# Performance work log

Hardware: AMD Instinct MI355X
Metric: run time of the kernel (lower is better)

## Reference

```python
import jax, jax.numpy as jnp
import numpy as np

E = 256   # in_features / embed_dim
O = 256   # out_features
H = 8     # n_heads
D = E // H  # head_dim
NEG = -1e9
SLOPE = 0.2  # leaky_relu negative slope


def setup_inputs() -> dict:
    key = jax.random.key(0)
    ks = jax.random.split(key, 9)
    B, N = 8, 1024
    x = jax.random.normal(ks[0], (B, N, E), dtype=jnp.float32)
    adj_matrix = jax.random.randint(ks[1], (N, N), 0, 2, dtype=jnp.int32)
    s = 1.0 / np.sqrt(E)
    w_in = jax.random.uniform(ks[2], (3 * E, E), jnp.float32, -s, s)   # packed q/k/v proj (torch in_proj_weight)
    b_in = jnp.zeros((3 * E,), jnp.float32)
    w_out = jax.random.uniform(ks[3], (E, E), jnp.float32, -s, s)      # MHA out_proj
    b_out = jnp.zeros((E,), jnp.float32)
    w_lin = jax.random.uniform(ks[4], (O, E), jnp.float32, -s, s)      # final nn.Linear
    b_lin = jax.random.uniform(ks[5], (O,), jnp.float32, -s, s)
    return {"x": x, "adj_matrix": adj_matrix, "w_in": w_in, "b_in": b_in,
            "w_out": w_out, "b_out": b_out, "w_lin": w_lin, "b_lin": b_lin}


def reference(x, adj_matrix, w_in, b_in, w_out, b_out, w_lin, b_lin):
    B, N, _ = x.shape
    scale = 1.0 / np.sqrt(D)
    qkv = x @ w_in.T + b_in                      # [B,N,3E]
    q, k, v = jnp.split(qkv, 3, axis=-1)
    q = q.reshape(B, N, H, D) * scale
    k = k.reshape(B, N, H, D)
    v = v.reshape(B, N, H, D)
    scores = jnp.einsum('bnhd,bmhd->bhnm', q, k)  # [B,H,N,N]
    allowed = (adj_matrix != 0)[None, None]       # mask True where adj==0 -> disallowed
    scores = jnp.where(allowed, scores, NEG)
    attn = jax.nn.softmax(scores, axis=-1)
    ctx = jnp.einsum('bhnm,bmhd->bnhd', attn, v).reshape(B, N, E)
    attended = ctx @ w_out.T + b_out              # MHA output (dropout is identity in eval)
    out = attended @ w_lin.T + b_lin
    return jnp.where(out >= 0, out, SLOPE * out)  # leaky_relu(0.2)
```

## Files before the change

### kernel.cpp

```cpp
#include <hip/hip_runtime.h>
#include <math.h>

#define EE 256
#define HH 8
#define DD 32
#define NB 8
#define NS 1024
#define SLOPE 0.2f

typedef float f32x4 __attribute__((ext_vector_type(4)));
typedef short short8 __attribute__((ext_vector_type(8)));

static __device__ __forceinline__ unsigned short f2b(float f) {
    unsigned int u = __float_as_uint(f);
    u = (u + 0x7FFFu + ((u >> 16) & 1u)) >> 16;
    return (unsigned short)u;
}

static __device__ __forceinline__ unsigned int cvtpk(float lo, float hi) {
    unsigned int r;
    asm("v_cvt_pk_bf16_f32 %0, %1, %2" : "=v"(r) : "v"(lo), "v"(hi));
    return r;
}

static __device__ __forceinline__ void gload_lds16(const void* g, void* l) {
    __builtin_amdgcn_global_load_lds(
        (const __attribute__((address_space(1))) unsigned int*)g,
        (__attribute__((address_space(3))) unsigned int*)l, 16, 0, 0);
}

__global__ __launch_bounds__(256) void cvt_all(const float* __restrict__ x,
                                               const float* __restrict__ wi,
                                               unsigned short* __restrict__ xb,
                                               unsigned short* __restrict__ wib) {
    int t = blockIdx.x * 256 + threadIdx.x;
    const float* src; unsigned short* dst; int base;
    if (t < 262144) { src = x;  dst = xb;  base = t; }
    else            { src = wi; dst = wib; base = t - 262144; }
    const float4* s = (const float4*)(src + (size_t)base * 8);
    float4 a = s[0], b = s[1];
    uint4 wv;
    wv.x = cvtpk(a.x, a.y); wv.y = cvtpk(a.z, a.w);
    wv.z = cvtpk(b.x, b.y); wv.w = cvtpk(b.z, b.w);
    *(uint4*)(dst + (size_t)base * 8) = wv;
}

__global__ __launch_bounds__(256) void make_comb(
    const float* __restrict__ wo, const float* __restrict__ bo,
    const float* __restrict__ wl, const float* __restrict__ bl,
    unsigned short* __restrict__ wcb, float* __restrict__ bcomb) {
    int o = blockIdx.x, c = threadIdx.x;
    const float* wlr = wl + (size_t)o * EE;
    float acc = 0.f;
#pragma unroll 8
    for (int e = 0; e < EE; ++e)
        acc = fmaf(wlr[e], wo[(size_t)e * EE + c], acc);
    wcb[(size_t)o * EE + c] = f2b(acc);
    if (c == 0) {
        float bb = bl[o];
        for (int e = 0; e < EE; ++e) bb = fmaf(wlr[e], bo[e], bb);
        bcomb[o] = bb;
    }
}

__global__ __launch_bounds__(256) void adj_to_bits(const int* __restrict__ adj,
                                                   unsigned int* __restrict__ bits) {
    int t = blockIdx.x * 256 + threadIdx.x;
    int n = t >> 5, w = t & 31;
    const int* p = adj + (size_t)n * NS + w * 32;
    unsigned int word = 0;
#pragma unroll
    for (int i = 0; i < 32; i += 4) {
        int4 a = *(const int4*)(p + i);
        if (a.x) word |= 1u << i;
        if (a.y) word |= 1u << (i + 1);
        if (a.z) word |= 1u << (i + 2);
        if (a.w) word |= 1u << (i + 3);
    }
    bits[t] = word;
}

template<int MODE>
__global__ __launch_bounds__(256) void gemm_mfma(
    const unsigned short* __restrict__ A, const unsigned short* __restrict__ W,
    const float* __restrict__ bias, void* __restrict__ out,
    unsigned short* __restrict__ qb, unsigned short* __restrict__ kb,
    unsigned short* __restrict__ vtb, int Nout) {
    __shared__ __align__(16) unsigned short As[128 * 64];
    __shared__ __align__(16) unsigned short Bs[64 * 64];
    int tid = threadIdx.x, w = tid >> 6, lane = tid & 63;
    int lq = lane & 15, g = lane >> 4;
    int wr = w >> 1, wc = w & 1;
    int m0 = blockIdx.y * 128, n0 = blockIdx.x * 64;
    int r8 = lane >> 3, c8 = (lane & 7) * 8;
    f32x4 acc[4][2];
#pragma unroll
    for (int i = 0; i < 4; ++i)
#pragma unroll
        for (int j = 0; j < 2; ++j) acc[i][j] = (f32x4){0.f, 0.f, 0.f, 0.f};

    for (int k0 = 0; k0 < 256; k0 += 64) {
        __syncthreads();
#pragma unroll
        for (int i = 0; i < 4; ++i)
            gload_lds16(A + (size_t)(m0 + w * 32 + i * 8 + r8) * 256 + k0 + c8,
                        &As[(w * 32 + i * 8) * 64]);
#pragma unroll
        for (int i = 0; i < 2; ++i)
            gload_lds16(W + (size_t)(n0 + w * 16 + i * 8 + r8) * 256 + k0 + c8,
                        &Bs[(w * 16 + i * 8) * 64]);
        __syncthreads();
#pragma unroll
        for (int ks = 0; ks < 2; ++ks) {
            short8 af[4], bf[2];
#pragma unroll
            for (int mi = 0; mi < 4; ++mi)
                af[mi] = *(const short8*)(&As[(wr * 64 + mi * 16 + lq) * 64 + ks * 32 + g * 8]);
#pragma unroll
            for (int ni = 0; ni < 2; ++ni)
                bf[ni] = *(const short8*)(&Bs[(wc * 32 + ni * 16 + lq) * 64 + ks * 32 + g * 8]);
#pragma unroll
            for (int mi = 0; mi < 4; ++mi)
#pragma unroll
                for (int ni = 0; ni < 2; ++ni)
                    acc[mi][ni] = __builtin_amdgcn_mfma_f32_16x16x32_bf16(af[mi], bf[ni], acc[mi][ni], 0, 0, 0);
        }
    }
    const float scale = 0.17677669529663687f;
#pragma unroll
    for (int mi = 0; mi < 4; ++mi) {
#pragma unroll
        for (int reg = 0; reg < 4; ++reg) {
            int m = m0 + wr * 64 + mi * 16 + g * 4 + reg;
#pragma unroll
            for (int ni = 0; ni < 2; ++ni) {
                int n = n0 + wc * 32 + ni * 16 + lq;
                float v = acc[mi][ni][reg] + bias[n];
                if (MODE == 1) {
                    v = v >= 0.f ? v : SLOPE * v;
                    ((float*)out)[(size_t)m * Nout + n] = v;
                } else {
                    int sec = n >> 8, cc = n & 255, h = cc >> 5, d = cc & 31;
                    int b = m >> 10, nr = m & (NS - 1);
                    if (sec == 0)
                        qb[((size_t)(b * HH + h) * NS + nr) * DD + d] = f2b(v * scale);
                    else if (sec == 1)
                        kb[((size_t)(b * HH + h) * NS + nr) * DD + d] = f2b(v);
                    else {
                        int nrp = (nr & ~31) | ((nr & 12) << 1) | ((nr & 16) >> 2) | (nr & 3);
                        vtb[((size_t)(b * HH + h) * DD + d) * NS + nrp] = f2b(v);
                    }
                }
            }
        }
    }
}

__global__ __launch_bounds__(256) void attn_mfma(
    const unsigned short* __restrict__ q, const unsigned short* __restrict__ k,
    const unsigned short* __restrict__ vt, const unsigned int* __restrict__ adjbits,
    unsigned short* __restrict__ ctx) {
    __shared__ __align__(16) unsigned short Ks[128 * 40];
    __shared__ __align__(16) unsigned short Vs[32 * 136];
    int tid = threadIdx.x;
    int w = tid >> 6, lane = tid & 63;
    int lq = lane & 15, g = lane >> 4;
    int bh = blockIdx.y;
    int n0 = blockIdx.x * 64;
    int nq = n0 + w * 16 + lq;
    const unsigned short* qb = q + (size_t)bh * NS * DD;
    const unsigned short* kb = k + (size_t)bh * NS * DD;
    const unsigned short* vb = vt + (size_t)bh * DD * NS;
    short8 qfrag = *(const short8*)(qb + (size_t)nq * DD + g * 8);
    const unsigned int* abr = adjbits + (size_t)nq * 32;
    float lsA = 0.f, lsB = 0.f;
    f32x4 acc0 = {0.f, 0.f, 0.f, 0.f}, acc1 = {0.f, 0.f, 0.f, 0.f};
    int kr = tid >> 1, kc = (tid & 1) * 16;
    int vd = tid >> 3, vc = (tid & 7) * 16;

    for (int m0 = 0; m0 < NS; m0 += 128) {
        __syncthreads();
        {
            const unsigned short* ksrc = kb + (size_t)(m0 + kr) * DD + kc;
            *(int4*)(&Ks[kr * 40 + kc])     = *(const int4*)(ksrc);
            *(int4*)(&Ks[kr * 40 + kc + 8]) = *(const int4*)(ksrc + 8);
            const unsigned short* vsrc = vb + (size_t)vd * NS + m0 + vc;
            *(int4*)(&Vs[vd * 136 + vc])     = *(const int4*)(vsrc);
            *(int4*)(&Vs[vd * 136 + vc + 8]) = *(const int4*)(vsrc + 8);
        }
        __syncthreads();

        uint4 w4 = *(const uint4*)(abr + (m0 >> 5));
        const f32x4 z = {0.f, 0.f, 0.f, 0.f};
#pragma unroll
        for (int T = 0; T < 4; ++T) {
            unsigned int wdT = (T == 0) ? w4.x : (T == 1) ? w4.y : (T == 2) ? w4.z : w4.w;
            short8 kf0 = *(const short8*)(&Ks[(32 * T + lq) * 40 + g * 8]);
            short8 kf1 = *(const short8*)(&Ks[(32 * T + 16 + lq) * 40 + g * 8]);
            f32x4 s0 = __builtin_amdgcn_mfma_f32_16x16x32_bf16(kf0, qfrag, z, 0, 0, 0);
            f32x4 s1 = __builtin_amdgcn_mfma_f32_16x16x32_bf16(kf1, qfrag, z, 0, 0, 0);
            unsigned int b0 = wdT >> (4 * g);
            unsigned int b1 = wdT >> (16 + 4 * g);
            float p0 = ((b0 >> 0) & 1u) ? __expf(s0[0]) : 0.f;
            float p1 = ((b0 >> 1) & 1u) ? __expf(s0[1]) : 0.f;
            float p2 = ((b0 >> 2) & 1u) ? __expf(s0[2]) : 0.f;
            float p3 = ((b0 >> 3) & 1u) ? __expf(s0[3]) : 0.f;
            float p4 = ((b1 >> 0) & 1u) ? __expf(s1[0]) : 0.f;
            float p5 = ((b1 >> 1) & 1u) ? __expf(s1[1]) : 0.f;
            float p6 = ((b1 >> 2) & 1u) ? __expf(s1[2]) : 0.f;
            float p7 = ((b1 >> 3) & 1u) ? __expf(s1[3]) : 0.f;
            lsA += (p0 + p1) + (p2 + p3);
            lsB += (p4 + p5) + (p6 + p7);
            union { uint4 u; short8 s; } pb;
            pb.u.x = cvtpk(p0, p1); pb.u.y = cvtpk(p2, p3);
            pb.u.z = cvtpk(p4, p5); pb.u.w = cvtpk(p6, p7);
            short8 va0 = *(const short8*)(&Vs[lq * 136 + T * 32 + g * 8]);
            short8 va1 = *(const short8*)(&Vs[(16 + lq) * 136 + T * 32 + g * 8]);
            acc0 = __builtin_amdgcn_mfma_f32_16x16x32_bf16(va0, pb.s, acc0, 0, 0, 0);
            acc1 = __builtin_amdgcn_mfma_f32_16x16x32_bf16(va1, pb.s, acc1, 0, 0, 0);
        }
    }
    float rs = lsA + lsB;
    rs += __shfl_xor(rs, 16);
    rs += __shfl_xor(rs, 32);
    float inv = 1.f / rs;
    int b = bh >> 3, h = bh & 7;
    unsigned short* dst = ctx + ((size_t)(b * NS + nq)) * EE + h * DD;
    uint2 o0, o1;
    o0.x = cvtpk(acc0[0] * inv, acc0[1] * inv);
    o0.y = cvtpk(acc0[2] * inv, acc0[3] * inv);
    o1.x = cvtpk(acc1[0] * inv, acc1[1] * inv);
    o1.y = cvtpk(acc1[2] * inv, acc1[3] * inv);
    *(uint2*)(dst + 4 * g) = o0;
    *(uint2*)(dst + 16 + 4 * g) = o1;
}

extern "C" void kernel_launch(void* const* d_in, const int* in_sizes, int n_in,
                              void* d_out, int out_size, void* d_ws, size_t ws_size,
                              hipStream_t stream) {
    const float* x     = (const float*)d_in[0];
    const int*   adj   = (const int*)d_in[1];
    const float* w_in  = (const float*)d_in[2];
    const float* b_in  = (const float*)d_in[3];
    const float* w_out = (const float*)d_in[4];
    const float* b_out = (const float*)d_in[5];
    const float* w_lin = (const float*)d_in[6];
    const float* b_lin = (const float*)d_in[7];
    float* out = (float*)d_out;

    const size_t S = (size_t)NB * HH * NS * DD;
    unsigned short* qb   = (unsigned short*)d_ws;
    unsigned short* kb   = qb + S;
    unsigned short* vtb  = kb + S;
    unsigned short* ctxb = vtb + S;
    unsigned short* xb   = ctxb + S;
    unsigned short* wib  = xb + S;
    unsigned short* wcb  = wib + 768 * 256;
    unsigned int* adjbits = (unsigned int*)(wcb + 256 * 256);
    float* bcomb = (float*)(adjbits + 32768);

    dim3 blk(256);
    cvt_all<<<dim3(1120), blk, 0, stream>>>(x, w_in, xb, wib);
    make_comb<<<dim3(256), blk, 0, stream>>>(w_out, b_out, w_lin, b_lin, wcb, bcomb);
    adj_to_bits<<<dim3((NS * 32) / 256), blk, 0, stream>>>(adj, adjbits);
    gemm_mfma<2><<<dim3(12, 64), blk, 0, stream>>>(xb, wib, b_in, nullptr, qb, kb, vtb, 768);
    attn_mfma<<<dim3(NS / 64, NB * HH), blk, 0, stream>>>(qb, kb, vtb, adjbits, ctxb);
    gemm_mfma<1><<<dim3(4, 64), blk, 0, stream>>>(ctxb, wcb, bcomb, out, nullptr, nullptr, nullptr, 256);
}
```

Before: 80.63 us.

## Merge prep kernels into one launch and double-buffer attention K/V tiles

Fuses the three preprocessing kernels (bf16 conversion, adjacency bitpacking, combined output weight) into one launch with block-range dispatch, which removes two launch gaps. The attention kernel now double-buffers its K/V shared-memory tiles: the next tile is prefetched into registers while MFMAs run on the current one, then stored to the other buffer. This cuts one barrier per iteration. It also raises wave priority around the compute section. Doubling the LDS use and holding prefetch registers may lower occupancy.

```diff
diff --git a/kernel.cpp b/kernel.cpp
--- a/kernel.cpp
+++ b/kernel.cpp
@@ -29,55 +29,54 @@
         (__attribute__((address_space(3))) unsigned int*)l, 16, 0, 0);
 }
 
-__global__ __launch_bounds__(256) void cvt_all(const float* __restrict__ x,
-                                               const float* __restrict__ wi,
-                                               unsigned short* __restrict__ xb,
-                                               unsigned short* __restrict__ wib) {
-    int t = blockIdx.x * 256 + threadIdx.x;
-    const float* src; unsigned short* dst; int base;
-    if (t < 262144) { src = x;  dst = xb;  base = t; }
-    else            { src = wi; dst = wib; base = t - 262144; }
-    const float4* s = (const float4*)(src + (size_t)base * 8);
-    float4 a = s[0], b = s[1];
-    uint4 wv;
-    wv.x = cvtpk(a.x, a.y); wv.y = cvtpk(a.z, a.w);
-    wv.z = cvtpk(b.x, b.y); wv.w = cvtpk(b.z, b.w);
-    *(uint4*)(dst + (size_t)base * 8) = wv;
-}
-
-__global__ __launch_bounds__(256) void make_comb(
+__global__ __launch_bounds__(256) void prep(
+    const float* __restrict__ x, const float* __restrict__ wi,
     const float* __restrict__ wo, const float* __restrict__ bo,
     const float* __restrict__ wl, const float* __restrict__ bl,
-    unsigned short* __restrict__ wcb, float* __restrict__ bcomb) {
-    int o = blockIdx.x, c = threadIdx.x;
-    const float* wlr = wl + (size_t)o * EE;
-    float acc = 0.f;
+    const int* __restrict__ adj,
+    unsigned short* __restrict__ xb, unsigned short* __restrict__ wib,
+    unsigned short* __restrict__ wcb, float* __restrict__ bcomb,
+    unsigned int* __restrict__ bits) {
+    int blk = blockIdx.x;
+    if (blk < 1120) {
+        int t = blk * 256 + threadIdx.x;
+        const float* src; unsigned short* dst; int base;
+        if (t < 262144) { src = x;  dst = xb;  base = t; }
+        else            { src = wi; dst = wib; base = t - 262144; }
+        const float4* s = (const float4*)(src + (size_t)base * 8);
+        float4 a = s[0], b = s[1];
+        uint4 wv;
+        wv.x = cvtpk(a.x, a.y); wv.y = cvtpk(a.z, a.w);
+        wv.z = cvtpk(b.x, b.y); wv.w = cvtpk(b.z, b.w);
+        *(uint4*)(dst + (size_t)base * 8) = wv;
+    } else if (blk < 1248) {
+        int t = (blk - 1120) * 256 + threadIdx.x;
+        int n = t >> 5, w = t & 31;
+        const int* p = adj + (size_t)n * NS + w * 32;
+        unsigned int word = 0;
+#pragma unroll
+        for (int i = 0; i < 32; i += 4) {
+            int4 a = *(const int4*)(p + i);
+            if (a.x) word |= 1u << i;
+            if (a.y) word |= 1u << (i + 1);
+            if (a.z) word |= 1u << (i + 2);
+            if (a.w) word |= 1u << (i + 3);
+        }
+        bits[t] = word;
+    } else {
+        int o = blk - 1248, c = threadIdx.x;
+        const float* wlr = wl + (size_t)o * EE;
+        float acc = 0.f;
 #pragma unroll 8
-    for (int e = 0; e < EE; ++e)
-        acc = fmaf(wlr[e], wo[(size_t)e * EE + c], acc);
-    wcb[(size_t)o * EE + c] = f2b(acc);
-    if (c == 0) {
-        float bb = bl[o];
-        for (int e = 0; e < EE; ++e) bb = fmaf(wlr[e], bo[e], bb);
-        bcomb[o] = bb;
-    }
-}
-
-__global__ __launch_bounds__(256) void adj_to_bits(const int* __restrict__ adj,
-                                                   unsigned int* __restrict__ bits) {
-    int t = blockIdx.x * 256 + threadIdx.x;
-    int n = t >> 5, w = t & 31;
-    const int* p = adj + (size_t)n * NS + w * 32;
-    unsigned int word = 0;
-#pragma unroll
-    for (int i = 0; i < 32; i += 4) {
-        int4 a = *(const int4*)(p + i);
-        if (a.x) word |= 1u << i;
-        if (a.y) word |= 1u << (i + 1);
-        if (a.z) word |= 1u << (i + 2);
-        if (a.w) word |= 1u << (i + 3);
-    }
-    bits[t] = word;
+        for (int e = 0; e < EE; ++e)
+            acc = fmaf(wlr[e], wo[(size_t)e * EE + c], acc);
+        wcb[(size_t)o * EE + c] = f2b(acc);
+        if (c == 0) {
+            float bb = bl[o];
+            for (int e = 0; e < EE; ++e) bb = fmaf(wlr[e], bo[e], bb);
+            bcomb[o] = bb;
+        }
+    }
 }
 
 template<int MODE>
@@ -160,8 +159,8 @@
     const unsigned short* __restrict__ q, const unsigned short* __restrict__ k,
     const unsigned short* __restrict__ vt, const unsigned int* __restrict__ adjbits,
     unsigned short* __restrict__ ctx) {
-    __shared__ __align__(16) unsigned short Ks[128 * 40];
-    __shared__ __align__(16) unsigned short Vs[32 * 136];
+    __shared__ __align__(16) unsigned short Ks[2][128 * 40];
+    __shared__ __align__(16) unsigned short Vs[2][32 * 136];
     int tid = threadIdx.x;
     int w = tid >> 6, lane = tid & 63;
     int lq = lane & 15, g = lane >> 4;
@@ -169,34 +168,47 @@
     int n0 = blockIdx.x * 64;
     int nq = n0 + w * 16 + lq;
     const unsigned short* qb = q + (size_t)bh * NS * DD;
-    const unsigned short* kb = k + (size_t)bh * NS * DD;
-    const unsigned short* vb = vt + (size_t)bh * DD * NS;
+    const unsigned short* kbp = k + (size_t)bh * NS * DD;
+    const unsigned short* vbp = vt + (size_t)bh * DD * NS;
     short8 qfrag = *(const short8*)(qb + (size_t)nq * DD + g * 8);
     const unsigned int* abr = adjbits + (size_t)nq * 32;
     float lsA = 0.f, lsB = 0.f;
     f32x4 acc0 = {0.f, 0.f, 0.f, 0.f}, acc1 = {0.f, 0.f, 0.f, 0.f};
     int kr = tid >> 1, kc = (tid & 1) * 16;
     int vd = tid >> 3, vc = (tid & 7) * 16;
-
-    for (int m0 = 0; m0 < NS; m0 += 128) {
-        __syncthreads();
-        {
-            const unsigned short* ksrc = kb + (size_t)(m0 + kr) * DD + kc;
-            *(int4*)(&Ks[kr * 40 + kc])     = *(const int4*)(ksrc);
-            *(int4*)(&Ks[kr * 40 + kc + 8]) = *(const int4*)(ksrc + 8);
-            const unsigned short* vsrc = vb + (size_t)vd * NS + m0 + vc;
-            *(int4*)(&Vs[vd * 136 + vc])     = *(const int4*)(vsrc);
-            *(int4*)(&Vs[vd * 136 + vc + 8]) = *(const int4*)(vsrc + 8);
-        }
-        __syncthreads();
-
-        uint4 w4 = *(const uint4*)(abr + (m0 >> 5));
+    const unsigned short* kst = kbp + (size_t)kr * DD + kc;
+    const unsigned short* vst = vbp + (size_t)vd * NS + vc;
+
+    int4 ka = *(const int4*)(kst);
+    int4 kb2 = *(const int4*)(kst + 8);
+    int4 va = *(const int4*)(vst);
+    int4 vb2 = *(const int4*)(vst + 8);
+    *(int4*)(&Ks[0][kr * 40 + kc])     = ka;
+    *(int4*)(&Ks[0][kr * 40 + kc + 8]) = kb2;
+    *(int4*)(&Vs[0][vd * 136 + vc])     = va;
+    *(int4*)(&Vs[0][vd * 136 + vc + 8]) = vb2;
+    __syncthreads();
+
+    int c = 0;
+    for (int t = 0; t < 8; ++t) {
+        if (t < 7) {
+            const unsigned short* kn = kst + (size_t)(t + 1) * 128 * DD;
+            const unsigned short* vn = vst + (size_t)(t + 1) * 128;
+            ka  = *(const int4*)(kn);
+            kb2 = *(const int4*)(kn + 8);
+            va  = *(const int4*)(vn);
+            vb2 = *(const int4*)(vn + 8);
+        }
+        const unsigned short* ksl = Ks[c];
+        const unsigned short* vsl = Vs[c];
+        uint4 w4 = *(const uint4*)(abr + t * 4);
         const f32x4 z = {0.f, 0.f, 0.f, 0.f};
+        __builtin_amdgcn_s_setprio(1);
 #pragma unroll
         for (int T = 0; T < 4; ++T) {
             unsigned int wdT = (T == 0) ? w4.x : (T == 1) ? w4.y : (T == 2) ? w4.z : w4.w;
-            short8 kf0 = *(const short8*)(&Ks[(32 * T + lq) * 40 + g * 8]);
-            short8 kf1 = *(const short8*)(&Ks[(32 * T + 16 + lq) * 40 + g * 8]);
+            short8 kf0 = *(const short8*)(&ksl[(32 * T + lq) * 40 + g * 8]);
+            short8 kf1 = *(const short8*)(&ksl[(32 * T + 16 + lq) * 40 + g * 8]);
             f32x4 s0 = __builtin_amdgcn_mfma_f32_16x16x32_bf16(kf0, qfrag, z, 0, 0, 0);
             f32x4 s1 = __builtin_amdgcn_mfma_f32_16x16x32_bf16(kf1, qfrag, z, 0, 0, 0);
             unsigned int b0 = wdT >> (4 * g);
@@ -214,11 +226,20 @@
             union { uint4 u; short8 s; } pb;
             pb.u.x = cvtpk(p0, p1); pb.u.y = cvtpk(p2, p3);
             pb.u.z = cvtpk(p4, p5); pb.u.w = cvtpk(p6, p7);
-            short8 va0 = *(const short8*)(&Vs[lq * 136 + T * 32 + g * 8]);
-            short8 va1 = *(const short8*)(&Vs[(16 + lq) * 136 + T * 32 + g * 8]);
+            short8 va0 = *(const short8*)(&vsl[lq * 136 + T * 32 + g * 8]);
+            short8 va1 = *(const short8*)(&vsl[(16 + lq) * 136 + T * 32 + g * 8]);
             acc0 = __builtin_amdgcn_mfma_f32_16x16x32_bf16(va0, pb.s, acc0, 0, 0, 0);
             acc1 = __builtin_amdgcn_mfma_f32_16x16x32_bf16(va1, pb.s, acc1, 0, 0, 0);
         }
+        __builtin_amdgcn_s_setprio(0);
+        if (t < 7) {
+            *(int4*)(&Ks[c ^ 1][kr * 40 + kc])     = ka;
+            *(int4*)(&Ks[c ^ 1][kr * 40 + kc + 8]) = kb2;
+            *(int4*)(&Vs[c ^ 1][vd * 136 + vc])     = va;
+            *(int4*)(&Vs[c ^ 1][vd * 136 + vc + 8]) = vb2;
+        }
+        __syncthreads();
+        c ^= 1;
     }
     float rs = lsA + lsB;
     rs += __shfl_xor(rs, 16);
@@ -260,9 +281,8 @@
     float* bcomb = (float*)(adjbits + 32768);
 
     dim3 blk(256);
-    cvt_all<<<dim3(1120), blk, 0, stream>>>(x, w_in, xb, wib);
-    make_comb<<<dim3(256), blk, 0, stream>>>(w_out, b_out, w_lin, b_lin, wcb, bcomb);
-    adj_to_bits<<<dim3((NS * 32) / 256), blk, 0, stream>>>(adj, adjbits);
+    prep<<<dim3(1504), blk, 0, stream>>>(x, w_in, w_out, b_out, w_lin, b_lin, adj,
+                                         xb, wib, wcb, bcomb, adjbits);
     gemm_mfma<2><<<dim3(12, 64), blk, 0, stream>>>(xb, wib, b_in, nullptr, qb, kb, vtb, 768);
     attn_mfma<<<dim3(NS / 64, NB * HH), blk, 0, stream>>>(qb, kb, vtb, adjbits, ctxb);
     gemm_mfma<1><<<dim3(4, 64), blk, 0, stream>>>(ctxb, wcb, bcomb, out, nullptr, nullptr, nullptr, 256);
```

Measured after the change: 72.34 us. 10.3% less time.
